# Optimization experiments

Measured on AMD Instinct MI355X. Metric: run time of the kernel, lower is better.

## Reference

```python
import jax, jax.numpy as jnp
import numpy as np

ALPHA = 0.2  # LeakyReLU negative slope
B, N, F_IN, F_OUT = 8, 2048, 256, 64


def setup_inputs() -> dict:
    key = jax.random.key(0)
    k1, k2, k3, k4 = jax.random.split(key, 4)
    x = jax.random.normal(k1, (B, N, F_IN), dtype=jnp.float32)
    adj = jax.random.randint(k2, (B, N, N), 0, 2, dtype=jnp.int32)
    # xavier_uniform with gain=1.414
    gain = 1.414
    lim_W = gain * np.sqrt(6.0 / (F_IN + F_OUT))
    W = jax.random.uniform(k3, (F_IN, F_OUT), dtype=jnp.float32, minval=-lim_W, maxval=lim_W)
    lim_a = gain * np.sqrt(6.0 / (2 * F_OUT + 1))
    a = jax.random.uniform(k4, (2 * F_OUT, 1), dtype=jnp.float32, minval=-lim_a, maxval=lim_a)
    return {"x": x, "adj": adj, "W": W, "a": a}


def reference(x, adj, W, a):
    h = jnp.einsum('bni,io->bno', x, W)  # [B, N, F_OUT]
    f_out = W.shape[1]
    # additive score a^T [h_i ; h_j] = (h_i . a_left) + (h_j . a_right)
    a_left = a[:f_out, 0]   # [F_OUT]
    a_right = a[f_out:, 0]  # [F_OUT]
    e_l = h @ a_left   # [B, N]
    e_r = h @ a_right  # [B, N]
    e = e_l[:, :, None] + e_r[:, None, :]          # [B, N, N]
    e = jnp.where(e > 0, e, ALPHA * e)             # LeakyReLU
    e = jnp.where(adj > 0, e, jnp.float32(-9e15))  # adjacency mask
    attention = jax.nn.softmax(e, axis=2)          # [B, N, N]
    h_prime = jnp.einsum('bnm,bmo->bno', attention, h)  # [B, N, F_OUT]
    return jax.nn.elu(h_prime)
```

## Files before the change

kernel.cpp:

```cpp
#include <hip/hip_runtime.h>
#include <math.h>

#define BATCH 8
#define NN 2048
#define FIN 256
#define FOUT 64
#define ALPHA 0.2f

typedef __attribute__((ext_vector_type(8))) short bf16x8;
typedef __attribute__((ext_vector_type(4))) float f32x4;

static __device__ __forceinline__ unsigned short f2bf(float f) {
  unsigned int u = __float_as_uint(f);
  u += 0x7fffu + ((u >> 16) & 1u);
  return (unsigned short)(u >> 16);
}
static __device__ __forceinline__ float bf2f(unsigned short h) {
  return __uint_as_float(((unsigned int)h) << 16);
}
static __device__ __forceinline__ void gload16(const void* g, void* l) {
  __builtin_amdgcn_global_load_lds(
      (const __attribute__((address_space(1))) unsigned int*)g,
      (__attribute__((address_space(3))) unsigned int*)l, 16, 0, 0);
}

__global__ __launch_bounds__(256) void k1_h(
    const float* __restrict__ x, const float* __restrict__ W,
    const float* __restrict__ a, float* __restrict__ el,
    float* __restrict__ er, unsigned char* __restrict__ hS) {
  __shared__ __align__(16) unsigned short lds[32768];
  const int t = threadIdx.x;
  const int wv = t >> 6;
  const int l = t & 63;
  const int l15 = l & 15;
  const int kg = l >> 4;

  {
    const float4* W4 = (const float4*)W;
    #pragma unroll
    for (int i = 0; i < 16; ++i) {
      int f = t + i * 256;
      float4 v = W4[f];
      int k = f >> 4;
      int ob = (f & 15) * 4;
      float vv[4] = {v.x, v.y, v.z, v.w};
      #pragma unroll
      for (int c = 0; c < 4; ++c) {
        int o = ob + c;
        unsigned short hi = f2bf(vv[c]);
        unsigned short lo = f2bf(vv[c] - bf2f(hi));
        int idx = o * 256 + (((k >> 3) ^ (o & 7)) * 8) + (k & 7);
        lds[idx] = hi;
        lds[16384 + idx] = lo;
      }
    }
  }
  __syncthreads();

  const int row = blockIdx.x * 64 + wv * 16 + l15;
  f32x4 acc[4] = {{0.f,0.f,0.f,0.f},{0.f,0.f,0.f,0.f},
                  {0.f,0.f,0.f,0.f},{0.f,0.f,0.f,0.f}};
  const float* xrow = x + (size_t)row * FIN;

  #pragma unroll
  for (int ks = 0; ks < 8; ++ks) {
    int k0 = ks * 32;
    float4 xa = *(const float4*)(xrow + k0 + kg * 8);
    float4 xb = *(const float4*)(xrow + k0 + kg * 8 + 4);
    float xv[8] = {xa.x, xa.y, xa.z, xa.w, xb.x, xb.y, xb.z, xb.w};
    bf16x8 ahi, alo;
    #pragma unroll
    for (int j = 0; j < 8; ++j) {
      unsigned short hi = f2bf(xv[j]);
      unsigned short lo = f2bf(xv[j] - bf2f(hi));
      ahi[j] = (short)hi;
      alo[j] = (short)lo;
    }
    int kgidx = ks * 4 + kg;
    #pragma unroll
    for (int ot = 0; ot < 4; ++ot) {
      int o = ot * 16 + l15;
      int base = o * 256 + ((kgidx ^ (o & 7)) * 8);
      bf16x8 bhi = *(const bf16x8*)&lds[base];
      bf16x8 blo = *(const bf16x8*)&lds[16384 + base];
      acc[ot] = __builtin_amdgcn_mfma_f32_16x16x32_bf16(ahi, bhi, acc[ot], 0, 0, 0);
      acc[ot] = __builtin_amdgcn_mfma_f32_16x16x32_bf16(ahi, blo, acc[ot], 0, 0, 0);
      acc[ot] = __builtin_amdgcn_mfma_f32_16x16x32_bf16(alo, bhi, acc[ot], 0, 0, 0);
    }
  }

  float aLv[4], aRv[4];
  #pragma unroll
  for (int ot = 0; ot < 4; ++ot) {
    aLv[ot] = a[ot * 16 + l15];
    aRv[ot] = a[64 + ot * 16 + l15];
  }
  #pragma unroll
  for (int jj = 0; jj < 4; ++jj) {
    float pl = 0.f, pr = 0.f;
    #pragma unroll
    for (int ot = 0; ot < 4; ++ot) {
      pl += acc[ot][jj] * aLv[ot];
      pr += acc[ot][jj] * aRv[ot];
    }
    #pragma unroll
    for (int s = 1; s < 16; s <<= 1) {
      pl += __shfl_xor(pl, s);
      pr += __shfl_xor(pr, s);
    }
    if (l15 == 0) {
      int grow = blockIdx.x * 64 + wv * 16 + kg * 4 + jj;
      el[grow] = pl;
      er[grow] = pr;
    }
  }

  __syncthreads();
  #pragma unroll
  for (int ot = 0; ot < 4; ++ot) {
    int o = ot * 16 + l15;
    int xorv = (o >> 1) & 3;
    #pragma unroll
    for (int jj = 0; jj < 4; ++jj) {
      int m_loc = wv * 16 + kg * 4 + jj;
      int ks2 = m_loc >> 5;
      int kg2 = (m_loc >> 3) & 3;
      int j = m_loc & 7;
      int kgp = kg2 ^ xorv;
      float v = acc[ot][jj];
      unsigned short hi = f2bf(v);
      unsigned short lo = f2bf(v - bf2f(hi));
      int base = ((ks2 * 2 + 0) * 64 + o) * 32 + kgp * 8 + j;
      lds[base] = hi;
      lds[base + 2048] = lo;
    }
  }
  __syncthreads();

  {
    const uint4* src = (const uint4*)(const void*)lds;
    uint4* dst = (uint4*)(hS + (size_t)blockIdx.x * 16384);
    #pragma unroll
    for (int i = 0; i < 4; ++i) dst[t + i * 256] = src[t + i * 256];
  }
}

__global__ __launch_bounds__(128) void k2_attn(
    const int* __restrict__ adj, const unsigned char* __restrict__ hS,
    const float* __restrict__ el, const float* __restrict__ er,
    float* __restrict__ out) {
  __shared__ __align__(1024) unsigned char buf[2][16384];
  const int t = threadIdx.x;
  const int wv = t >> 6;
  const int l = t & 63;
  const int l15 = l & 15;
  const int kg = l >> 4;

  int bid = blockIdx.x;
  int swz = (bid & 7) * 64 + (bid >> 3);
  int b = swz >> 6;
  int n0 = (swz & 63) * 32;
  const int nrow = n0 + wv * 16 + l15;

  const float eL = el[b * NN + nrow];
  const float* erb = er + b * NN;
  const int* arow = adj + (size_t)b * NN * NN + (size_t)nrow * NN;
  const unsigned char* hSb = hS + (size_t)b * 32 * 16384;

  const int laneoff = l15 * 64 + ((kg ^ ((l >> 1) & 3)) * 16);

  f32x4 acc[4] = {{0.f,0.f,0.f,0.f},{0.f,0.f,0.f,0.f},
                  {0.f,0.f,0.f,0.f},{0.f,0.f,0.f,0.f}};
  float Sacc = 0.f;

  #pragma unroll
  for (int s = 0; s < 8; ++s) {
    int seg = wv * 8 + s;
    gload16(hSb + seg * 1024 + l * 16, &buf[0][seg * 1024]);
  }
  int4 av[4];
  float4 ev[4];
  #pragma unroll
  for (int ksx = 0; ksx < 2; ++ksx) {
    av[ksx * 2 + 0] = *(const int4*)(arow + ksx * 32 + kg * 8);
    av[ksx * 2 + 1] = *(const int4*)(arow + ksx * 32 + kg * 8 + 4);
    ev[ksx * 2 + 0] = *(const float4*)(erb + ksx * 32 + kg * 8);
    ev[ksx * 2 + 1] = *(const float4*)(erb + ksx * 32 + kg * 8 + 4);
  }
  __syncthreads();

  for (int tc = 0; tc < 32; ++tc) {
    const unsigned char* cur = buf[tc & 1];
    int4 avn[4];
    float4 evn[4];
    if (tc < 31) {
      const unsigned char* src = hSb + (size_t)(tc + 1) * 16384;
      unsigned char* dstb = buf[(tc + 1) & 1];
      #pragma unroll
      for (int s = 0; s < 8; ++s) {
        int seg = wv * 8 + s;
        gload16(src + seg * 1024 + l * 16, dstb + seg * 1024);
      }
      int mb = (tc + 1) * 64;
      #pragma unroll
      for (int ksx = 0; ksx < 2; ++ksx) {
        avn[ksx * 2 + 0] = *(const int4*)(arow + mb + ksx * 32 + kg * 8);
        avn[ksx * 2 + 1] = *(const int4*)(arow + mb + ksx * 32 + kg * 8 + 4);
        evn[ksx * 2 + 0] = *(const float4*)(erb + mb + ksx * 32 + kg * 8);
        evn[ksx * 2 + 1] = *(const float4*)(erb + mb + ksx * 32 + kg * 8 + 4);
      }
    }

    #pragma unroll
    for (int ks = 0; ks < 2; ++ks) {
      int aarr[8] = {av[ks*2].x, av[ks*2].y, av[ks*2].z, av[ks*2].w,
                     av[ks*2+1].x, av[ks*2+1].y, av[ks*2+1].z, av[ks*2+1].w};
      float earr[8] = {ev[ks*2].x, ev[ks*2].y, ev[ks*2].z, ev[ks*2].w,
                       ev[ks*2+1].x, ev[ks*2+1].y, ev[ks*2+1].z, ev[ks*2+1].w};
      bf16x8 af;
      #pragma unroll
      for (int j = 0; j < 8; ++j) {
        float e = eL + earr[j];
        e = fmaxf(e, ALPHA * e);
        float w = (aarr[j] > 0) ? __expf(e) : 0.f;
        unsigned short hb = f2bf(w);
        af[j] = (short)hb;
        Sacc += bf2f(hb);
      }
      #pragma unroll
      for (int ot = 0; ot < 4; ++ot) {
        const unsigned char* p = cur + ks * 8192 + ot * 1024 + laneoff;
        bf16x8 bhi = *(const bf16x8*)p;
        bf16x8 blo = *(const bf16x8*)(p + 4096);
        acc[ot] = __builtin_amdgcn_mfma_f32_16x16x32_bf16(af, bhi, acc[ot], 0, 0, 0);
        acc[ot] = __builtin_amdgcn_mfma_f32_16x16x32_bf16(af, blo, acc[ot], 0, 0, 0);
      }
    }

    if (tc < 31) {
      #pragma unroll
      for (int i = 0; i < 4; ++i) { av[i] = avn[i]; ev[i] = evn[i]; }
    }
    __syncthreads();
  }

  float Sred = Sacc + __shfl_xor(Sacc, 16);
  Sred += __shfl_xor(Sred, 32);
  float Sj[4];
  #pragma unroll
  for (int jj = 0; jj < 4; ++jj) Sj[jj] = __shfl(Sred, kg * 4 + jj);
  #pragma unroll
  for (int ot = 0; ot < 4; ++ot) {
    #pragma unroll
    for (int jj = 0; jj < 4; ++jj) {
      float v = acc[ot][jj] / Sj[jj];
      float res = v > 0.f ? v : expm1f(v);
      out[((size_t)b * NN + n0 + wv * 16 + kg * 4 + jj) * FOUT + ot * 16 + l15] = res;
    }
  }
}

extern "C" void kernel_launch(void* const* d_in, const int* in_sizes, int n_in,
                              void* d_out, int out_size, void* d_ws, size_t ws_size,
                              hipStream_t stream) {
  const float* x   = (const float*)d_in[0];
  const int*   adj = (const int*)d_in[1];
  const float* W   = (const float*)d_in[2];
  const float* a   = (const float*)d_in[3];
  float* out = (float*)d_out;

  unsigned char* hS = (unsigned char*)d_ws;
  float* el = (float*)(hS + (size_t)BATCH * 32 * 16384);
  float* er = el + BATCH * NN;

  hipLaunchKernelGGL(k1_h, dim3(256), dim3(256), 0, stream, x, W, a, el, er, hS);
  hipLaunchKernelGGL(k2_attn, dim3(512), dim3(128), 0, stream, adj, hS, el, er, out);
}
```

Baseline: 61.18 us.

## Split attention key dimension across two wave pairs with LDS reduction

Each block now runs four waves instead of two. The two wave pairs each process half of the key (m) dimension with their own double-buffered LDS staging of h, then combine partial accumulators and row sums through shared memory before normalisation and ELU. This doubles the waves in flight per block and halves the serial loop length, aiming to hide memory latency on the adjacency stream. The cost is double the LDS per block, a final LDS reduction and an extra barrier, which may lower occupancy.

```diff
diff --git a/kernel.cpp b/kernel.cpp
--- a/kernel.cpp
+++ b/kernel.cpp
@@ -145,27 +145,30 @@
   }
 }
 
-__global__ __launch_bounds__(128) void k2_attn(
+__global__ __launch_bounds__(256, 2) void k2_attn(
     const int* __restrict__ adj, const unsigned char* __restrict__ hS,
     const float* __restrict__ el, const float* __restrict__ er,
     float* __restrict__ out) {
-  __shared__ __align__(1024) unsigned char buf[2][16384];
+  __shared__ __align__(1024) unsigned char buf[2][2][16384];
   const int t = threadIdx.x;
   const int wv = t >> 6;
   const int l = t & 63;
   const int l15 = l & 15;
   const int kg = l >> 4;
+  const int pair = wv >> 1;
+  const int pw = wv & 1;
 
   int bid = blockIdx.x;
   int swz = (bid & 7) * 64 + (bid >> 3);
   int b = swz >> 6;
   int n0 = (swz & 63) * 32;
-  const int nrow = n0 + wv * 16 + l15;
+  const int nrow = n0 + pw * 16 + l15;
 
   const float eL = el[b * NN + nrow];
-  const float* erb = er + b * NN;
-  const int* arow = adj + (size_t)b * NN * NN + (size_t)nrow * NN;
-  const unsigned char* hSb = hS + (size_t)b * 32 * 16384;
+  const float* erp = er + b * NN + pair * 1024;
+  const int* arow = adj + (size_t)b * NN * NN + (size_t)nrow * NN + pair * 1024;
+  const unsigned char* hSb =
+      hS + (size_t)b * 32 * 16384 + (size_t)pair * 16 * 16384;
 
   const int laneoff = l15 * 64 + ((kg ^ ((l >> 1) & 3)) * 16);
 
@@ -175,8 +178,8 @@
 
   #pragma unroll
   for (int s = 0; s < 8; ++s) {
-    int seg = wv * 8 + s;
-    gload16(hSb + seg * 1024 + l * 16, &buf[0][seg * 1024]);
+    int seg = pw * 8 + s;
+    gload16(hSb + seg * 1024 + l * 16, &buf[pair][0][seg * 1024]);
   }
   int4 av[4];
   float4 ev[4];
@@ -184,21 +187,21 @@
   for (int ksx = 0; ksx < 2; ++ksx) {
     av[ksx * 2 + 0] = *(const int4*)(arow + ksx * 32 + kg * 8);
     av[ksx * 2 + 1] = *(const int4*)(arow + ksx * 32 + kg * 8 + 4);
-    ev[ksx * 2 + 0] = *(const float4*)(erb + ksx * 32 + kg * 8);
-    ev[ksx * 2 + 1] = *(const float4*)(erb + ksx * 32 + kg * 8 + 4);
+    ev[ksx * 2 + 0] = *(const float4*)(erp + ksx * 32 + kg * 8);
+    ev[ksx * 2 + 1] = *(const float4*)(erp + ksx * 32 + kg * 8 + 4);
   }
   __syncthreads();
 
-  for (int tc = 0; tc < 32; ++tc) {
-    const unsigned char* cur = buf[tc & 1];
+  for (int tc = 0; tc < 16; ++tc) {
+    const unsigned char* cur = &buf[pair][tc & 1][0];
     int4 avn[4];
     float4 evn[4];
-    if (tc < 31) {
+    if (tc < 15) {
       const unsigned char* src = hSb + (size_t)(tc + 1) * 16384;
-      unsigned char* dstb = buf[(tc + 1) & 1];
+      unsigned char* dstb = &buf[pair][(tc + 1) & 1][0];
       #pragma unroll
       for (int s = 0; s < 8; ++s) {
-        int seg = wv * 8 + s;
+        int seg = pw * 8 + s;
         gload16(src + seg * 1024 + l * 16, dstb + seg * 1024);
       }
       int mb = (tc + 1) * 64;
@@ -206,8 +209,8 @@
       for (int ksx = 0; ksx < 2; ++ksx) {
         avn[ksx * 2 + 0] = *(const int4*)(arow + mb + ksx * 32 + kg * 8);
         avn[ksx * 2 + 1] = *(const int4*)(arow + mb + ksx * 32 + kg * 8 + 4);
-        evn[ksx * 2 + 0] = *(const float4*)(erb + mb + ksx * 32 + kg * 8);
-        evn[ksx * 2 + 1] = *(const float4*)(erb + mb + ksx * 32 + kg * 8 + 4);
+        evn[ksx * 2 + 0] = *(const float4*)(erp + mb + ksx * 32 + kg * 8);
+        evn[ksx * 2 + 1] = *(const float4*)(erp + mb + ksx * 32 + kg * 8 + 4);
       }
     }
 
@@ -237,7 +240,7 @@
       }
     }
 
-    if (tc < 31) {
+    if (tc < 15) {
       #pragma unroll
       for (int i = 0; i < 4; ++i) { av[i] = avn[i]; ev[i] = evn[i]; }
     }
@@ -246,6 +249,29 @@
 
   float Sred = Sacc + __shfl_xor(Sacc, 16);
   Sred += __shfl_xor(Sred, 32);
+
+  {
+    unsigned char* cb = &buf[0][0][0];
+    const int slot = pw * 64 + l;
+    if (pair == 1) {
+      float* dst = (float*)(cb + slot * 96);
+      *(f32x4*)(dst + 0)  = acc[0];
+      *(f32x4*)(dst + 4)  = acc[1];
+      *(f32x4*)(dst + 8)  = acc[2];
+      *(f32x4*)(dst + 12) = acc[3];
+      dst[16] = Sred;
+    }
+    __syncthreads();
+    if (pair == 1) return;
+    const float* src = (const float*)(cb + slot * 96);
+    #pragma unroll
+    for (int ot = 0; ot < 4; ++ot) {
+      f32x4 o4 = *(const f32x4*)(src + ot * 4);
+      acc[ot] += o4;
+    }
+    Sred += src[16];
+  }
+
   float Sj[4];
   #pragma unroll
   for (int jj = 0; jj < 4; ++jj) Sj[jj] = __shfl(Sred, kg * 4 + jj);
@@ -255,7 +281,7 @@
     for (int jj = 0; jj < 4; ++jj) {
       float v = acc[ot][jj] / Sj[jj];
       float res = v > 0.f ? v : expm1f(v);
-      out[((size_t)b * NN + n0 + wv * 16 + kg * 4 + jj) * FOUT + ot * 16 + l15] = res;
+      out[((size_t)b * NN + n0 + pw * 16 + kg * 4 + jj) * FOUT + ot * 16 + l15] = res;
     }
   }
 }
@@ -274,5 +300,5 @@
   float* er = el + BATCH * NN;
 
   hipLaunchKernelGGL(k1_h, dim3(256), dim3(256), 0, stream, x, W, a, el, er, hS);
-  hipLaunchKernelGGL(k2_attn, dim3(512), dim3(128), 0, stream, adj, hS, el, er, out);
-}
+  hipLaunchKernelGGL(k2_attn, dim3(512), dim3(256), 0, stream, adj, hS, el, er, out);
+}
```

Result: faster. 52.57 us (-14.1%).

## Split attention K-dimension across four waves with per-wave pipelines and LDS reduction

Applied to the files above, without the earlier changes.

The attention kernel now runs four waves per block. Each wave owns a quarter of the neighbour columns for both 16-row tiles, instead of each wave owning one row tile across all columns. Each wave streams its own hS slice through a private double buffer and keeps a three-deep register prefetch of adj and er. Block-wide barriers in the loop are replaced by explicit vmcnt waits, and partial accumulators and row sums are reduced through LDS at the end. It also adds a low-order bf16 term for the attention weights (three MFMAs per tile instead of two) to improve accuracy, at the cost of extra MFMA work and more registers.

```diff
diff --git a/kernel.cpp b/kernel.cpp
--- a/kernel.cpp
+++ b/kernel.cpp
@@ -145,11 +145,11 @@
   }
 }
 
-__global__ __launch_bounds__(128) void k2_attn(
+__global__ __launch_bounds__(256, 2) void k2_attn(
     const int* __restrict__ adj, const unsigned char* __restrict__ hS,
     const float* __restrict__ el, const float* __restrict__ er,
     float* __restrict__ out) {
-  __shared__ __align__(1024) unsigned char buf[2][16384];
+  __shared__ __align__(1024) unsigned char buf[4][2][8192];
   const int t = threadIdx.x;
   const int wv = t >> 6;
   const int l = t & 63;
@@ -160,102 +160,152 @@
   int swz = (bid & 7) * 64 + (bid >> 3);
   int b = swz >> 6;
   int n0 = (swz & 63) * 32;
-  const int nrow = n0 + wv * 16 + l15;
-
-  const float eL = el[b * NN + nrow];
-  const float* erb = er + b * NN;
-  const int* arow = adj + (size_t)b * NN * NN + (size_t)nrow * NN;
-  const unsigned char* hSb = hS + (size_t)b * 32 * 16384;
+
+  const int row0 = n0 + l15;
+  const int row1 = n0 + 16 + l15;
+  const float eL0 = el[b * NN + row0];
+  const float eL1 = el[b * NN + row1];
+  const int* arow0 = adj + (size_t)b * NN * NN + (size_t)row0 * NN + wv * 512;
+  const int* arow1 = adj + (size_t)b * NN * NN + (size_t)row1 * NN + wv * 512;
+  const float* erp = er + b * NN + wv * 512;
+  const unsigned char* hW = hS + (size_t)b * 32 * 16384 + (size_t)wv * 16 * 8192;
 
   const int laneoff = l15 * 64 + ((kg ^ ((l >> 1) & 3)) * 16);
 
-  f32x4 acc[4] = {{0.f,0.f,0.f,0.f},{0.f,0.f,0.f,0.f},
-                  {0.f,0.f,0.f,0.f},{0.f,0.f,0.f,0.f}};
-  float Sacc = 0.f;
-
-  #pragma unroll
-  for (int s = 0; s < 8; ++s) {
-    int seg = wv * 8 + s;
-    gload16(hSb + seg * 1024 + l * 16, &buf[0][seg * 1024]);
-  }
-  int4 av[4];
-  float4 ev[4];
-  #pragma unroll
-  for (int ksx = 0; ksx < 2; ++ksx) {
-    av[ksx * 2 + 0] = *(const int4*)(arow + ksx * 32 + kg * 8);
-    av[ksx * 2 + 1] = *(const int4*)(arow + ksx * 32 + kg * 8 + 4);
-    ev[ksx * 2 + 0] = *(const float4*)(erb + ksx * 32 + kg * 8);
-    ev[ksx * 2 + 1] = *(const float4*)(erb + ksx * 32 + kg * 8 + 4);
-  }
-  __syncthreads();
-
-  for (int tc = 0; tc < 32; ++tc) {
-    const unsigned char* cur = buf[tc & 1];
-    int4 avn[4];
-    float4 evn[4];
-    if (tc < 31) {
-      const unsigned char* src = hSb + (size_t)(tc + 1) * 16384;
-      unsigned char* dstb = buf[(tc + 1) & 1];
-      #pragma unroll
-      for (int s = 0; s < 8; ++s) {
-        int seg = wv * 8 + s;
-        gload16(src + seg * 1024 + l * 16, dstb + seg * 1024);
-      }
-      int mb = (tc + 1) * 64;
-      #pragma unroll
-      for (int ksx = 0; ksx < 2; ++ksx) {
-        avn[ksx * 2 + 0] = *(const int4*)(arow + mb + ksx * 32 + kg * 8);
-        avn[ksx * 2 + 1] = *(const int4*)(arow + mb + ksx * 32 + kg * 8 + 4);
-        evn[ksx * 2 + 0] = *(const float4*)(erb + mb + ksx * 32 + kg * 8);
-        evn[ksx * 2 + 1] = *(const float4*)(erb + mb + ksx * 32 + kg * 8 + 4);
-      }
-    }
-
-    #pragma unroll
-    for (int ks = 0; ks < 2; ++ks) {
-      int aarr[8] = {av[ks*2].x, av[ks*2].y, av[ks*2].z, av[ks*2].w,
-                     av[ks*2+1].x, av[ks*2+1].y, av[ks*2+1].z, av[ks*2+1].w};
-      float earr[8] = {ev[ks*2].x, ev[ks*2].y, ev[ks*2].z, ev[ks*2].w,
-                       ev[ks*2+1].x, ev[ks*2+1].y, ev[ks*2+1].z, ev[ks*2+1].w};
-      bf16x8 af;
-      #pragma unroll
-      for (int j = 0; j < 8; ++j) {
-        float e = eL + earr[j];
-        e = fmaxf(e, ALPHA * e);
-        float w = (aarr[j] > 0) ? __expf(e) : 0.f;
-        unsigned short hb = f2bf(w);
-        af[j] = (short)hb;
-        Sacc += bf2f(hb);
-      }
-      #pragma unroll
-      for (int ot = 0; ot < 4; ++ot) {
-        const unsigned char* p = cur + ks * 8192 + ot * 1024 + laneoff;
-        bf16x8 bhi = *(const bf16x8*)p;
-        bf16x8 blo = *(const bf16x8*)(p + 4096);
-        acc[ot] = __builtin_amdgcn_mfma_f32_16x16x32_bf16(af, bhi, acc[ot], 0, 0, 0);
-        acc[ot] = __builtin_amdgcn_mfma_f32_16x16x32_bf16(af, blo, acc[ot], 0, 0, 0);
-      }
-    }
-
-    if (tc < 31) {
-      #pragma unroll
-      for (int i = 0; i < 4; ++i) { av[i] = avn[i]; ev[i] = evn[i]; }
-    }
-    __syncthreads();
-  }
-
-  float Sred = Sacc + __shfl_xor(Sacc, 16);
-  Sred += __shfl_xor(Sred, 32);
-  float Sj[4];
-  #pragma unroll
-  for (int jj = 0; jj < 4; ++jj) Sj[jj] = __shfl(Sred, kg * 4 + jj);
+  f32x4 acc[2][4] = {{{0.f,0.f,0.f,0.f},{0.f,0.f,0.f,0.f},
+                      {0.f,0.f,0.f,0.f},{0.f,0.f,0.f,0.f}},
+                     {{0.f,0.f,0.f,0.f},{0.f,0.f,0.f,0.f},
+                      {0.f,0.f,0.f,0.f},{0.f,0.f,0.f,0.f}}};
+  float S0 = 0.f, S1 = 0.f;
+
+  int4 av[3][4];
+  float4 ev[3][2];
+
+#define STAGE(cc) {                                                        \
+    const unsigned char* src_ = hW + (size_t)(cc) * 8192;                  \
+    unsigned char* dst_ = &buf[wv][(cc) & 1][0];                           \
+    _Pragma("unroll")                                                      \
+    for (int s_ = 0; s_ < 8; ++s_)                                         \
+      gload16(src_ + s_ * 1024 + l * 16, dst_ + s_ * 1024);                \
+  }
+#define LOADR(slot, cc) {                                                  \
+    int mb_ = (cc) * 32;                                                   \
+    av[slot][0] = *(const int4*)(arow0 + mb_ + kg * 8);                    \
+    av[slot][1] = *(const int4*)(arow0 + mb_ + kg * 8 + 4);                \
+    av[slot][2] = *(const int4*)(arow1 + mb_ + kg * 8);                    \
+    av[slot][3] = *(const int4*)(arow1 + mb_ + kg * 8 + 4);                \
+    ev[slot][0] = *(const float4*)(erp + mb_ + kg * 8);                    \
+    ev[slot][1] = *(const float4*)(erp + mb_ + kg * 8 + 4);                \
+  }
+
+  STAGE(0);
+  LOADR(0, 0);
+  LOADR(1, 1);
+
+  #pragma unroll
+  for (int c = 0; c < 16; ++c) {
+    if (c < 15) STAGE(c + 1);
+    if (c < 14) LOADR((c + 2) % 3, c + 2);
+
+    if (c < 14)      { asm volatile("s_waitcnt vmcnt(14)" ::: "memory"); }
+    else if (c < 15) { asm volatile("s_waitcnt vmcnt(8)"  ::: "memory"); }
+    else             { asm volatile("s_waitcnt vmcnt(0)"  ::: "memory"); }
+
+    const int sl = c % 3;
+    int a0[8] = {av[sl][0].x, av[sl][0].y, av[sl][0].z, av[sl][0].w,
+                 av[sl][1].x, av[sl][1].y, av[sl][1].z, av[sl][1].w};
+    int a1[8] = {av[sl][2].x, av[sl][2].y, av[sl][2].z, av[sl][2].w,
+                 av[sl][3].x, av[sl][3].y, av[sl][3].z, av[sl][3].w};
+    float ee[8] = {ev[sl][0].x, ev[sl][0].y, ev[sl][0].z, ev[sl][0].w,
+                   ev[sl][1].x, ev[sl][1].y, ev[sl][1].z, ev[sl][1].w};
+
+    bf16x8 af0h, af0l, af1h, af1l;
+    #pragma unroll
+    for (int j = 0; j < 8; ++j) {
+      float e0 = eL0 + ee[j];
+      e0 = fmaxf(e0, ALPHA * e0);
+      float w0 = (a0[j] > 0) ? __expf(e0) : 0.f;
+      unsigned short h0 = f2bf(w0);
+      float w0h = bf2f(h0);
+      unsigned short l0 = f2bf(w0 - w0h);
+      af0h[j] = (short)h0;
+      af0l[j] = (short)l0;
+      S0 += w0h + bf2f(l0);
+
+      float e1 = eL1 + ee[j];
+      e1 = fmaxf(e1, ALPHA * e1);
+      float w1 = (a1[j] > 0) ? __expf(e1) : 0.f;
+      unsigned short h1 = f2bf(w1);
+      float w1h = bf2f(h1);
+      unsigned short l1 = f2bf(w1 - w1h);
+      af1h[j] = (short)h1;
+      af1l[j] = (short)l1;
+      S1 += w1h + bf2f(l1);
+    }
+
+    const unsigned char* cur = &buf[wv][c & 1][0];
+    #pragma unroll
+    for (int ot = 0; ot < 4; ++ot) {
+      const unsigned char* p = cur + ot * 1024 + laneoff;
+      bf16x8 bhi = *(const bf16x8*)p;
+      bf16x8 blo = *(const bf16x8*)(p + 4096);
+      acc[0][ot] = __builtin_amdgcn_mfma_f32_16x16x32_bf16(af0h, bhi, acc[0][ot], 0, 0, 0);
+      acc[0][ot] = __builtin_amdgcn_mfma_f32_16x16x32_bf16(af0h, blo, acc[0][ot], 0, 0, 0);
+      acc[0][ot] = __builtin_amdgcn_mfma_f32_16x16x32_bf16(af0l, bhi, acc[0][ot], 0, 0, 0);
+      acc[1][ot] = __builtin_amdgcn_mfma_f32_16x16x32_bf16(af1h, bhi, acc[1][ot], 0, 0, 0);
+      acc[1][ot] = __builtin_amdgcn_mfma_f32_16x16x32_bf16(af1h, blo, acc[1][ot], 0, 0, 0);
+      acc[1][ot] = __builtin_amdgcn_mfma_f32_16x16x32_bf16(af1l, bhi, acc[1][ot], 0, 0, 0);
+    }
+  }
+#undef STAGE
+#undef LOADR
+
+  S0 += __shfl_xor(S0, 16); S0 += __shfl_xor(S0, 32);
+  S1 += __shfl_xor(S1, 16); S1 += __shfl_xor(S1, 32);
+
+  __syncthreads();
+  float* cb = (float*)(void*)&buf[0][0][0];
+  if (wv > 0) {
+    float* dst = cb + ((wv - 1) * 64 + l) * 36;
+    #pragma unroll
+    for (int ot = 0; ot < 4; ++ot) {
+      *(f32x4*)(dst + ot * 4)      = acc[0][ot];
+      *(f32x4*)(dst + 16 + ot * 4) = acc[1][ot];
+    }
+    dst[32] = S0;
+    dst[33] = S1;
+  }
+  __syncthreads();
+  if (wv != 0) return;
+
+  #pragma unroll
+  for (int p = 0; p < 3; ++p) {
+    const float* src = cb + (p * 64 + l) * 36;
+    #pragma unroll
+    for (int ot = 0; ot < 4; ++ot) {
+      acc[0][ot] += *(const f32x4*)(src + ot * 4);
+      acc[1][ot] += *(const f32x4*)(src + 16 + ot * 4);
+    }
+    S0 += src[32];
+    S1 += src[33];
+  }
+
+  float Sj0[4], Sj1[4];
+  #pragma unroll
+  for (int jj = 0; jj < 4; ++jj) {
+    Sj0[jj] = __shfl(S0, kg * 4 + jj);
+    Sj1[jj] = __shfl(S1, kg * 4 + jj);
+  }
   #pragma unroll
   for (int ot = 0; ot < 4; ++ot) {
     #pragma unroll
     for (int jj = 0; jj < 4; ++jj) {
-      float v = acc[ot][jj] / Sj[jj];
-      float res = v > 0.f ? v : expm1f(v);
-      out[((size_t)b * NN + n0 + wv * 16 + kg * 4 + jj) * FOUT + ot * 16 + l15] = res;
+      float v0 = acc[0][ot][jj] / Sj0[jj];
+      float r0 = v0 > 0.f ? v0 : expm1f(v0);
+      out[((size_t)b * NN + n0 + kg * 4 + jj) * FOUT + ot * 16 + l15] = r0;
+      float v1 = acc[1][ot][jj] / Sj1[jj];
+      float r1 = v1 > 0.f ? v1 : expm1f(v1);
+      out[((size_t)b * NN + n0 + 16 + kg * 4 + jj) * FOUT + ot * 16 + l15] = r1;
     }
   }
 }
@@ -274,5 +324,5 @@
   float* er = el + BATCH * NN;
 
   hipLaunchKernelGGL(k1_h, dim3(256), dim3(256), 0, stream, x, W, a, el, er, hS);
-  hipLaunchKernelGGL(k2_attn, dim3(512), dim3(128), 0, stream, adj, hS, el, er, out);
-}
+  hipLaunchKernelGGL(k2_attn, dim3(512), dim3(256), 0, stream, adj, hS, el, er, out);
+}
```

Measured after the change: 50.65 us. 17.2% less time.

## Split attention K-dimension across waves with direct global B loads and LDS reduction

Applied to the files above, without the earlier changes.

The attention kernel now gives each block 16 rows, with its four waves each covering a quarter of the neighbour dimension. Each wave reads h fragments straight from global memory into registers and prefetches adjacency rows several steps ahead, replacing the LDS double-buffering and its per-iteration barriers. Partial accumulators and row sums are combined through a small LDS buffer at the end. The attention weights are also split into hi/lo bf16 parts, giving three MFMAs per tile for better precision. That adds tensor work, and h is now re-read from global or cache by every block.

```diff
diff --git a/kernel.cpp b/kernel.cpp
--- a/kernel.cpp
+++ b/kernel.cpp
@@ -17,11 +17,6 @@
 }
 static __device__ __forceinline__ float bf2f(unsigned short h) {
   return __uint_as_float(((unsigned int)h) << 16);
-}
-static __device__ __forceinline__ void gload16(const void* g, void* l) {
-  __builtin_amdgcn_global_load_lds(
-      (const __attribute__((address_space(1))) unsigned int*)g,
-      (__attribute__((address_space(3))) unsigned int*)l, 16, 0, 0);
 }
 
 __global__ __launch_bounds__(256) void k1_h(
@@ -145,11 +140,11 @@
   }
 }
 
-__global__ __launch_bounds__(128) void k2_attn(
+__global__ __launch_bounds__(256, 3) void k2_attn(
     const int* __restrict__ adj, const unsigned char* __restrict__ hS,
     const float* __restrict__ el, const float* __restrict__ er,
     float* __restrict__ out) {
-  __shared__ __align__(1024) unsigned char buf[2][16384];
+  __shared__ __align__(16) float cb[3 * 64 * 20];
   const int t = threadIdx.x;
   const int wv = t >> 6;
   const int l = t & 63;
@@ -157,105 +152,113 @@
   const int kg = l >> 4;
 
   int bid = blockIdx.x;
-  int swz = (bid & 7) * 64 + (bid >> 3);
-  int b = swz >> 6;
-  int n0 = (swz & 63) * 32;
-  const int nrow = n0 + wv * 16 + l15;
-
-  const float eL = el[b * NN + nrow];
-  const float* erb = er + b * NN;
-  const int* arow = adj + (size_t)b * NN * NN + (size_t)nrow * NN;
-  const unsigned char* hSb = hS + (size_t)b * 32 * 16384;
-
+  int swz = (bid & 7) * 128 + (bid >> 3);
+  int b = swz >> 7;
+  int n0 = (swz & 127) * 16;
+
+  const int row = n0 + l15;
+  const float eL = el[b * NN + row];
+  const int* arow = adj + (size_t)b * NN * NN + (size_t)row * NN + wv * 512;
+  const float* erp = er + b * NN + wv * 512;
+  const unsigned char* hW = hS + (size_t)b * 32 * 16384 + (size_t)wv * 16 * 8192;
   const int laneoff = l15 * 64 + ((kg ^ ((l >> 1) & 3)) * 16);
 
   f32x4 acc[4] = {{0.f,0.f,0.f,0.f},{0.f,0.f,0.f,0.f},
                   {0.f,0.f,0.f,0.f},{0.f,0.f,0.f,0.f}};
-  float Sacc = 0.f;
-
-  #pragma unroll
-  for (int s = 0; s < 8; ++s) {
-    int seg = wv * 8 + s;
-    gload16(hSb + seg * 1024 + l * 16, &buf[0][seg * 1024]);
-  }
-  int4 av[4];
-  float4 ev[4];
-  #pragma unroll
-  for (int ksx = 0; ksx < 2; ++ksx) {
-    av[ksx * 2 + 0] = *(const int4*)(arow + ksx * 32 + kg * 8);
-    av[ksx * 2 + 1] = *(const int4*)(arow + ksx * 32 + kg * 8 + 4);
-    ev[ksx * 2 + 0] = *(const float4*)(erb + ksx * 32 + kg * 8);
-    ev[ksx * 2 + 1] = *(const float4*)(erb + ksx * 32 + kg * 8 + 4);
-  }
-  __syncthreads();
-
-  for (int tc = 0; tc < 32; ++tc) {
-    const unsigned char* cur = buf[tc & 1];
-    int4 avn[4];
-    float4 evn[4];
-    if (tc < 31) {
-      const unsigned char* src = hSb + (size_t)(tc + 1) * 16384;
-      unsigned char* dstb = buf[(tc + 1) & 1];
-      #pragma unroll
-      for (int s = 0; s < 8; ++s) {
-        int seg = wv * 8 + s;
-        gload16(src + seg * 1024 + l * 16, dstb + seg * 1024);
-      }
-      int mb = (tc + 1) * 64;
-      #pragma unroll
-      for (int ksx = 0; ksx < 2; ++ksx) {
-        avn[ksx * 2 + 0] = *(const int4*)(arow + mb + ksx * 32 + kg * 8);
-        avn[ksx * 2 + 1] = *(const int4*)(arow + mb + ksx * 32 + kg * 8 + 4);
-        evn[ksx * 2 + 0] = *(const float4*)(erb + mb + ksx * 32 + kg * 8);
-        evn[ksx * 2 + 1] = *(const float4*)(erb + mb + ksx * 32 + kg * 8 + 4);
-      }
-    }
-
-    #pragma unroll
-    for (int ks = 0; ks < 2; ++ks) {
-      int aarr[8] = {av[ks*2].x, av[ks*2].y, av[ks*2].z, av[ks*2].w,
-                     av[ks*2+1].x, av[ks*2+1].y, av[ks*2+1].z, av[ks*2+1].w};
-      float earr[8] = {ev[ks*2].x, ev[ks*2].y, ev[ks*2].z, ev[ks*2].w,
-                       ev[ks*2+1].x, ev[ks*2+1].y, ev[ks*2+1].z, ev[ks*2+1].w};
-      bf16x8 af;
-      #pragma unroll
-      for (int j = 0; j < 8; ++j) {
-        float e = eL + earr[j];
-        e = fmaxf(e, ALPHA * e);
-        float w = (aarr[j] > 0) ? __expf(e) : 0.f;
-        unsigned short hb = f2bf(w);
-        af[j] = (short)hb;
-        Sacc += bf2f(hb);
-      }
+  float S = 0.f;
+
+  int4 av[3][2];
+  float4 evc0, evc1, evn0, evn1;
+
+  av[0][0] = *(const int4*)(arow + kg * 8);
+  av[0][1] = *(const int4*)(arow + kg * 8 + 4);
+  av[1][0] = *(const int4*)(arow + 32 + kg * 8);
+  av[1][1] = *(const int4*)(arow + 32 + kg * 8 + 4);
+  evc0 = *(const float4*)(erp + kg * 8);
+  evc1 = *(const float4*)(erp + kg * 8 + 4);
+
+  #pragma unroll
+  for (int c = 0; c < 16; ++c) {
+    bf16x8 curH[4], curL[4];
+    {
+      const unsigned char* p_ = hW + (size_t)c * 8192 + laneoff;
       #pragma unroll
       for (int ot = 0; ot < 4; ++ot) {
-        const unsigned char* p = cur + ks * 8192 + ot * 1024 + laneoff;
-        bf16x8 bhi = *(const bf16x8*)p;
-        bf16x8 blo = *(const bf16x8*)(p + 4096);
-        acc[ot] = __builtin_amdgcn_mfma_f32_16x16x32_bf16(af, bhi, acc[ot], 0, 0, 0);
-        acc[ot] = __builtin_amdgcn_mfma_f32_16x16x32_bf16(af, blo, acc[ot], 0, 0, 0);
+        curH[ot] = *(const bf16x8*)(p_ + ot * 1024);
+        curL[ot] = *(const bf16x8*)(p_ + ot * 1024 + 4096);
       }
     }
-
-    if (tc < 31) {
-      #pragma unroll
-      for (int i = 0; i < 4; ++i) { av[i] = avn[i]; ev[i] = evn[i]; }
-    }
-    __syncthreads();
-  }
-
-  float Sred = Sacc + __shfl_xor(Sacc, 16);
-  Sred += __shfl_xor(Sred, 32);
+    if (c < 14) {
+      int mb = (c + 2) * 32;
+      av[(c + 2) % 3][0] = *(const int4*)(arow + mb + kg * 8);
+      av[(c + 2) % 3][1] = *(const int4*)(arow + mb + kg * 8 + 4);
+    }
+    if (c < 15) {
+      evn0 = *(const float4*)(erp + (c + 1) * 32 + kg * 8);
+      evn1 = *(const float4*)(erp + (c + 1) * 32 + kg * 8 + 4);
+    }
+
+    const int sl = c % 3;
+    int a0[8] = {av[sl][0].x, av[sl][0].y, av[sl][0].z, av[sl][0].w,
+                 av[sl][1].x, av[sl][1].y, av[sl][1].z, av[sl][1].w};
+    float ee[8] = {evc0.x, evc0.y, evc0.z, evc0.w,
+                   evc1.x, evc1.y, evc1.z, evc1.w};
+
+    bf16x8 afh, afl;
+    #pragma unroll
+    for (int j = 0; j < 8; ++j) {
+      float e0 = eL + ee[j];
+      e0 = fmaxf(e0, ALPHA * e0);
+      float w0 = (a0[j] > 0) ? __expf(e0) : 0.f;
+      unsigned short h0 = f2bf(w0);
+      float w0h = bf2f(h0);
+      unsigned short l0 = f2bf(w0 - w0h);
+      afh[j] = (short)h0;
+      afl[j] = (short)l0;
+      S += w0h + bf2f(l0);
+    }
+
+    #pragma unroll
+    for (int ot = 0; ot < 4; ++ot) {
+      acc[ot] = __builtin_amdgcn_mfma_f32_16x16x32_bf16(afh, curH[ot], acc[ot], 0, 0, 0);
+      acc[ot] = __builtin_amdgcn_mfma_f32_16x16x32_bf16(afh, curL[ot], acc[ot], 0, 0, 0);
+      acc[ot] = __builtin_amdgcn_mfma_f32_16x16x32_bf16(afl, curH[ot], acc[ot], 0, 0, 0);
+    }
+
+    if (c < 15) { evc0 = evn0; evc1 = evn1; }
+  }
+
+  S += __shfl_xor(S, 16);
+  S += __shfl_xor(S, 32);
+
+  __syncthreads();
+  if (wv > 0) {
+    float* dst = cb + ((wv - 1) * 64 + l) * 20;
+    #pragma unroll
+    for (int ot = 0; ot < 4; ++ot) *(f32x4*)(dst + ot * 4) = acc[ot];
+    dst[16] = S;
+  }
+  __syncthreads();
+  if (wv != 0) return;
+
+  #pragma unroll
+  for (int p = 0; p < 3; ++p) {
+    const float* src = cb + (p * 64 + l) * 20;
+    #pragma unroll
+    for (int ot = 0; ot < 4; ++ot) acc[ot] += *(const f32x4*)(src + ot * 4);
+    S += src[16];
+  }
+
   float Sj[4];
   #pragma unroll
-  for (int jj = 0; jj < 4; ++jj) Sj[jj] = __shfl(Sred, kg * 4 + jj);
+  for (int jj = 0; jj < 4; ++jj) Sj[jj] = __shfl(S, kg * 4 + jj);
   #pragma unroll
   for (int ot = 0; ot < 4; ++ot) {
     #pragma unroll
     for (int jj = 0; jj < 4; ++jj) {
       float v = acc[ot][jj] / Sj[jj];
-      float res = v > 0.f ? v : expm1f(v);
-      out[((size_t)b * NN + n0 + wv * 16 + kg * 4 + jj) * FOUT + ot * 16 + l15] = res;
+      float r = v > 0.f ? v : expm1f(v);
+      out[((size_t)b * NN + n0 + kg * 4 + jj) * FOUT + ot * 16 + l15] = r;
     }
   }
 }
@@ -274,5 +277,5 @@
   float* er = el + BATCH * NN;
 
   hipLaunchKernelGGL(k1_h, dim3(256), dim3(256), 0, stream, x, W, a, el, er, hS);
-  hipLaunchKernelGGL(k2_attn, dim3(512), dim3(128), 0, stream, adj, hS, el, er, out);
-}
+  hipLaunchKernelGGL(k2_attn, dim3(1024), dim3(256), 0, stream, adj, hS, el, er, out);
+}
```

Measured after the change: 57.12 us. 6.6% less time.
